# Optimization experiments

Measured on AMD Instinct MI355X. Metric: run time of the kernel, lower is better.

Reference implementation:

```python
import jax, jax.numpy as jnp
import numpy as np

B, F, S, D = 256, 8, 200, 64
H = 36  # hidden units per field
EPS = 1e-3  # Dice BN epsilon


def setup_inputs() -> dict:
    key0 = jax.random.key(0)
    ks = jax.random.split(key0, 8)
    query = jax.random.normal(ks[0], (B, F, D), dtype=jnp.float32)
    key = jax.random.normal(ks[1], (B, F, S, D), dtype=jnp.float32)
    sequence_num = jax.random.randint(ks[2], (B, F), 1, S + 1, dtype=jnp.int32)
    W_h = jax.random.normal(ks[3], (F, 3 * D, H), dtype=jnp.float32) * 0.05
    b_h = jnp.zeros((F, H), dtype=jnp.float32)
    alpha = jnp.zeros((F,), dtype=jnp.float32)
    W_o = jax.random.normal(ks[4], (F, H, 1), dtype=jnp.float32) * 0.05
    b_o = jnp.zeros((F, 1), dtype=jnp.float32)
    return {"query": query, "key": key, "W_h": W_h, "b_h": b_h,
            "alpha": alpha, "W_o": W_o, "b_o": b_o,
            "sequence_num": sequence_num, "training": 1}


def reference(query, key, W_h, b_h, alpha, W_o, b_o, sequence_num, training):
    # query: [B,F,D], key: [B,F,S,D]
    q = query[:, :, None, :]                      # broadcast instead of tile
    qb = jnp.broadcast_to(q, key.shape)           # [B,F,S,D]
    cat = jnp.concatenate([key, qb, q - key], axis=-1)  # [B,F,S,3D]
    # per-field Dense(36), vectorized across fields
    h = jnp.einsum('bfsc,fch->bfsh', cat, W_h) + b_h[None, :, None, :]
    # Dice: BatchNorm (no affine, training-mode batch stats over batch+seq per field/feature)
    mean = h.mean(axis=(0, 2), keepdims=True)
    var = h.var(axis=(0, 2), keepdims=True)
    p = jax.nn.sigmoid((h - mean) * jax.lax.rsqrt(var + EPS))
    h = (alpha[None, :, None, None] * (1.0 - p) + p) * h
    # per-field Dense(1) -> attention scores [B,F,S]
    scores = jnp.einsum('bfsh,fh->bfs', h, W_o[:, :, 0]) + b_o[None, :, 0, None]
    # mask invalid positions and softmax over sequence
    mask = jnp.arange(key.shape[2])[None, None, :] < sequence_num[:, :, None]
    scores = jnp.where(mask, scores, -jnp.inf)
    attn = jax.nn.softmax(scores, axis=-1)        # [B,F,S]
    # weighted sum over sequence -> [B,F,D]
    return jnp.einsum('bfs,bfsd->bfd', attn, key)
```

## Files before the change

### kernel.cpp

```cpp
#include <hip/hip_runtime.h>
#include <math.h>

#define NB 256
#define NF 8
#define NS 200
#define ND 64
#define NH 36
#define EPSV 1e-3f

#define WS_SUM 0
#define WS_SQ  288
#define WS_QT  1152

typedef __attribute__((ext_vector_type(8))) short short8;
typedef __attribute__((ext_vector_type(4))) float f32x4;
typedef __attribute__((ext_vector_type(4))) int int4v;

__device__ __forceinline__ unsigned short f32_to_bf16_rne(float x) {
    unsigned u = __float_as_uint(x);
    unsigned r = u + 0x7FFFu + ((u >> 16) & 1u);
    return (unsigned short)(r >> 16);
}
__device__ __forceinline__ short8 pack8(float4 a, float4 b) {
    int4v t;
    t[0] = (int)__builtin_amdgcn_perm(__float_as_uint(a.y), __float_as_uint(a.x), 0x07060302u);
    t[1] = (int)__builtin_amdgcn_perm(__float_as_uint(a.w), __float_as_uint(a.z), 0x07060302u);
    t[2] = (int)__builtin_amdgcn_perm(__float_as_uint(b.y), __float_as_uint(b.x), 0x07060302u);
    t[3] = (int)__builtin_amdgcn_perm(__float_as_uint(b.w), __float_as_uint(b.z), 0x07060302u);
    return __builtin_bit_cast(short8, t);
}

__global__ __launch_bounds__(128, 4) void k_stats(
    const float* __restrict__ query, const float* __restrict__ key,
    const float* __restrict__ W_h, const float* __restrict__ b_h,
    float* __restrict__ ws)
{
    const int blk = blockIdx.x;
    const int f = blk & (NF - 1);
    const int tid = threadIdx.x;
    const int lane = tid & 63, wv = tid >> 6;
    const int col = lane & 15, quad = lane >> 4;

    __shared__ __align__(16) unsigned short wkL[48 * 72];
    __shared__ float qsL[64];
    __shared__ float qtL[48];
    __shared__ float s1L[2][48], s2L[2][48];

    const float* Wf = W_h + (size_t)f * (3 * ND * NH);
    const float* kbase = key + (size_t)blk * (NS * ND);

    float4 cur[4], nxt[4];
    {
        const int s = min(16 * wv + col, NS - 1);
        const float4* p = (const float4*)(kbase + (size_t)s * ND + quad * 8);
        cur[0] = p[0]; cur[1] = p[1]; cur[2] = p[8]; cur[3] = p[9];
    }
    if (tid < 64) qsL[tid] = query[(size_t)blk * ND + tid];
    for (int i = tid; i < 48 * 64; i += 128) {
        int h = i >> 6, d = i & 63;
        float v = (h < NH) ? (Wf[d * NH + h] - Wf[(2 * ND + d) * NH + h]) : 0.f;
        wkL[h * 72 + d] = f32_to_bf16_rne(v);
    }
    __syncthreads();

    short8 bfr[3][2];
    #pragma unroll
    for (int nt = 0; nt < 3; ++nt)
        #pragma unroll
        for (int ks = 0; ks < 2; ++ks)
            bfr[nt][ks] = *(const short8*)&wkL[(nt * 16 + col) * 72 + ks * 32 + quad * 8];

    float s1[3] = {0.f, 0.f, 0.f}, s2[3] = {0.f, 0.f, 0.f};
    #pragma unroll
    for (int t = 0; t < 7; ++t) {
        const int mt = wv + 2 * t;
        if (t < 6) {
            const int sn = min(16 * (mt + 2) + col, NS - 1);
            const float4* p = (const float4*)(kbase + (size_t)sn * ND + quad * 8);
            nxt[0] = p[0]; nxt[1] = p[1]; nxt[2] = p[8]; nxt[3] = p[9];
        }
        const short8 fa = pack8(cur[0], cur[1]);
        const short8 fb = pack8(cur[2], cur[3]);
        const int base_s = 16 * mt + quad * 4;
        #pragma unroll
        for (int nt = 0; nt < 3; ++nt) {
            f32x4 acc = {0.f, 0.f, 0.f, 0.f};
            acc = __builtin_amdgcn_mfma_f32_16x16x32_bf16(fa, bfr[nt][0], acc, 0, 0, 0);
            acc = __builtin_amdgcn_mfma_f32_16x16x32_bf16(fb, bfr[nt][1], acc, 0, 0, 0);
            #pragma unroll
            for (int r = 0; r < 4; ++r) {
                const float v = (base_s + r < NS) ? acc[r] : 0.f;
                s1[nt] += v; s2[nt] += v * v;
            }
        }
        cur[0] = nxt[0]; cur[1] = nxt[1]; cur[2] = nxt[2]; cur[3] = nxt[3];
    }

    if (tid >= 64 && tid < 64 + NH) {
        const int h = tid - 64;
        float acc = b_h[f * NH + h];
        #pragma unroll 8
        for (int d = 0; d < ND; ++d)
            acc += qsL[d] * (Wf[(ND + d) * NH + h] + Wf[(2 * ND + d) * NH + h]);
        qtL[h] = acc;
        ws[WS_QT + (size_t)blk * 48 + h] = acc;
    }
    if (tid >= 64 + NH && tid < 64 + 48)
        ws[WS_QT + (size_t)blk * 48 + (tid - 64)] = 0.f;

    #pragma unroll
    for (int nt = 0; nt < 3; ++nt) {
        float a = s1[nt], c = s2[nt];
        a += __shfl_xor(a, 16, 64); a += __shfl_xor(a, 32, 64);
        c += __shfl_xor(c, 16, 64); c += __shfl_xor(c, 32, 64);
        if (quad == 0) { s1L[wv][nt * 16 + col] = a; s2L[wv][nt * 16 + col] = c; }
    }
    __syncthreads();
    if (tid < NH) {
        const float S1 = s1L[0][tid] + s1L[1][tid];
        const float S2 = s2L[0][tid] + s2L[1][tid];
        const float qt = qtL[tid];
        atomicAdd(&ws[WS_SUM + f * NH + tid], S1 + 200.f * qt);
        atomicAdd(&ws[WS_SQ  + f * NH + tid], S2 + 2.f * qt * S1 + 200.f * qt * qt);
    }
}

__global__ __launch_bounds__(128, 4) void k_attn(
    const float* __restrict__ key, const float* __restrict__ W_h,
    const float* __restrict__ alpha, const float* __restrict__ W_o,
    const float* __restrict__ b_o, const int* __restrict__ seqn,
    const float* __restrict__ ws, float* __restrict__ out)
{
    const int blk = blockIdx.x;
    const int f = blk & (NF - 1);
    const int tid = threadIdx.x;
    const int lane = tid & 63, wv = tid >> 6;
    const int col = lane & 15, quad = lane >> 4;

    __shared__ __align__(16) unsigned short wkL[48 * 72];
    __shared__ float swL[208];
    __shared__ float redA[2], redB[2];
    __shared__ float poutL[2][64];

    const float* Wf = W_h + (size_t)f * (3 * ND * NH);
    const float* kbase = key + (size_t)blk * (NS * ND);

    float4 cur[4], nxt[4];
    {
        const int s = min(16 * wv + col, NS - 1);
        const float4* p = (const float4*)(kbase + (size_t)s * ND + quad * 8);
        cur[0] = p[0]; cur[1] = p[1]; cur[2] = p[8]; cur[3] = p[9];
    }
    for (int i = tid; i < 48 * 64; i += 128) {
        int h = i >> 6, d = i & 63;
        float v = (h < NH) ? (Wf[d * NH + h] - Wf[(2 * ND + d) * NH + h]) : 0.f;
        wkL[h * 72 + d] = f32_to_bf16_rne(v);
    }
    __syncthreads();

    short8 bfr[3][2];
    #pragma unroll
    for (int nt = 0; nt < 3; ++nt)
        #pragma unroll
        for (int ks = 0; ks < 2; ++ks)
            bfr[nt][ks] = *(const short8*)&wkL[(nt * 16 + col) * 72 + ks * 32 + quad * 8];

    const float inv_n = 1.f / (float)(NB * NS);
    float qv[3], mn[3], iv[3], wo[3];
    #pragma unroll
    for (int nt = 0; nt < 3; ++nt) {
        const int hh = nt * 16 + col;
        const bool hv = hh < NH;
        const int hc = hv ? hh : 0;
        qv[nt] = ws[WS_QT + (size_t)blk * 48 + hh];
        const float sm = ws[WS_SUM + f * NH + hc];
        const float sq = ws[WS_SQ  + f * NH + hc];
        const float m = sm * inv_n;
        mn[nt] = m;
        iv[nt] = rsqrtf(fmaxf(sq * inv_n - m * m, 0.f) + EPSV);
        wo[nt] = hv ? W_o[f * NH + hh] : 0.f;
    }
    const float alf = alpha[f];
    const float bo = b_o[f];
    const int sq_n = seqn[blk];

    #pragma unroll
    for (int t = 0; t < 7; ++t) {
        const int mt = wv + 2 * t;
        if (t < 6) {
            const int sn = min(16 * (mt + 2) + col, NS - 1);
            const float4* p = (const float4*)(kbase + (size_t)sn * ND + quad * 8);
            nxt[0] = p[0]; nxt[1] = p[1]; nxt[2] = p[8]; nxt[3] = p[9];
        }
        const short8 fa = pack8(cur[0], cur[1]);
        const short8 fb = pack8(cur[2], cur[3]);
        float part[4] = {0.f, 0.f, 0.f, 0.f};
        #pragma unroll
        for (int nt = 0; nt < 3; ++nt) {
            f32x4 acc = {qv[nt], qv[nt], qv[nt], qv[nt]};
            acc = __builtin_amdgcn_mfma_f32_16x16x32_bf16(fa, bfr[nt][0], acc, 0, 0, 0);
            acc = __builtin_amdgcn_mfma_f32_16x16x32_bf16(fb, bfr[nt][1], acc, 0, 0, 0);
            #pragma unroll
            for (int r = 0; r < 4; ++r) {
                const float h = acc[r];
                const float pg = 1.f / (1.f + __expf(-(h - mn[nt]) * iv[nt]));
                part[r] += (alf + (1.f - alf) * pg) * h * wo[nt];
            }
        }
        #pragma unroll
        for (int r = 0; r < 4; ++r) {
            float v = part[r];
            v += __shfl_xor(v, 1, 64); v += __shfl_xor(v, 2, 64);
            v += __shfl_xor(v, 4, 64); v += __shfl_xor(v, 8, 64);
            const int srow = 16 * mt + quad * 4 + r;
            if (col == 0 && srow < NS) swL[srow] = v + bo;
        }
        cur[0] = nxt[0]; cur[1] = nxt[1]; cur[2] = nxt[2]; cur[3] = nxt[3];
    }
    __syncthreads();

    const int i2 = tid + 128;
    const float v1 = (tid < sq_n) ? swL[tid] : -1e30f;
    const float v2 = (i2 < NS && i2 < sq_n) ? swL[i2] : -1e30f;
    float m = fmaxf(v1, v2);
    m = fmaxf(m, __shfl_xor(m, 1, 64));  m = fmaxf(m, __shfl_xor(m, 2, 64));
    m = fmaxf(m, __shfl_xor(m, 4, 64));  m = fmaxf(m, __shfl_xor(m, 8, 64));
    m = fmaxf(m, __shfl_xor(m, 16, 64)); m = fmaxf(m, __shfl_xor(m, 32, 64));
    if (lane == 0) redA[wv] = m;
    __syncthreads();
    const float maxv = fmaxf(redA[0], redA[1]);
    const float e1 = (tid < sq_n) ? __expf(v1 - maxv) : 0.f;
    const float e2 = (i2 < NS && i2 < sq_n) ? __expf(v2 - maxv) : 0.f;
    float l = e1 + e2;
    l += __shfl_xor(l, 1, 64);  l += __shfl_xor(l, 2, 64);
    l += __shfl_xor(l, 4, 64);  l += __shfl_xor(l, 8, 64);
    l += __shfl_xor(l, 16, 64); l += __shfl_xor(l, 32, 64);
    if (lane == 0) redB[wv] = l;
    __syncthreads();
    const float isum = 1.f / (redB[0] + redB[1]);
    swL[tid] = e1 * isum;
    if (i2 < 208) swL[i2] = e2 * isum;
    __syncthreads();

    {
        const int d = lane;
        float acc = 0.f;
        const int s0 = wv * 100;
        #pragma unroll 10
        for (int s = s0; s < s0 + 100; ++s)
            acc += swL[s] * kbase[(size_t)s * ND + d];
        poutL[wv][d] = acc;
    }
    __syncthreads();
    if (tid < 64)
        out[(size_t)blk * ND + tid] = poutL[0][tid] + poutL[1][tid];
}

extern "C" void kernel_launch(void* const* d_in, const int* in_sizes, int n_in,
                              void* d_out, int out_size, void* d_ws, size_t ws_size,
                              hipStream_t stream) {
    const float* query = (const float*)d_in[0];
    const float* key   = (const float*)d_in[1];
    const float* W_h   = (const float*)d_in[2];
    const float* b_h   = (const float*)d_in[3];
    const float* alpha = (const float*)d_in[4];
    const float* W_o   = (const float*)d_in[5];
    const float* b_o   = (const float*)d_in[6];
    const int*   seqn  = (const int*)d_in[7];
    float* out = (float*)d_out;
    float* ws  = (float*)d_ws;

    hipMemsetAsync(ws, 0, 576 * sizeof(float), stream);
    k_stats<<<NB * NF, 128, 0, stream>>>(query, key, W_h, b_h, ws);
    k_attn<<<NB * NF, 128, 0, stream>>>(key, W_h, alpha, W_o, b_o, seqn, ws, out);
}
```

Before: 225.7 us.

## Stage key tile in LDS as bf16, widen blocks, replace atomics with reduce kernel

After: 222.1 us. No clear change (-1.6%).

```diff
diff --git a/kernel.cpp b/kernel.cpp
--- a/kernel.cpp
+++ b/kernel.cpp
@@ -10,53 +10,63 @@
 
 #define WS_SUM 0
 #define WS_SQ  288
-#define WS_QT  1152
+#define WS_QT  4096
+#define WS_P   102400
 
 typedef __attribute__((ext_vector_type(8))) short short8;
 typedef __attribute__((ext_vector_type(4))) float f32x4;
-typedef __attribute__((ext_vector_type(4))) int int4v;
 
 __device__ __forceinline__ unsigned short f32_to_bf16_rne(float x) {
     unsigned u = __float_as_uint(x);
     unsigned r = u + 0x7FFFu + ((u >> 16) & 1u);
     return (unsigned short)(r >> 16);
 }
-__device__ __forceinline__ short8 pack8(float4 a, float4 b) {
-    int4v t;
-    t[0] = (int)__builtin_amdgcn_perm(__float_as_uint(a.y), __float_as_uint(a.x), 0x07060302u);
-    t[1] = (int)__builtin_amdgcn_perm(__float_as_uint(a.w), __float_as_uint(a.z), 0x07060302u);
-    t[2] = (int)__builtin_amdgcn_perm(__float_as_uint(b.y), __float_as_uint(b.x), 0x07060302u);
-    t[3] = (int)__builtin_amdgcn_perm(__float_as_uint(b.w), __float_as_uint(b.z), 0x07060302u);
-    return __builtin_bit_cast(short8, t);
-}
-
-__global__ __launch_bounds__(128, 4) void k_stats(
+__device__ __forceinline__ unsigned pack2(float x, float y) {
+    return __builtin_amdgcn_perm(__float_as_uint(y), __float_as_uint(x), 0x07060302u);
+}
+
+__device__ __forceinline__ void stage_key(const float* kbase, unsigned short* kL,
+                                          int tid, int lane, int wv) {
+    const float4* kb4 = (const float4*)kbase;
+    const int base = wv * 800;
+    #pragma unroll
+    for (int j = 0; j < 13; ++j) {
+        const int idx = base + j * 64 + lane;
+        const bool ok = (j < 12) | (lane < 32);
+        const float4 v = kb4[ok ? idx : base];
+        if (ok) {
+            const int r = idx >> 4, dc = idx & 15;
+            unsigned t0 = pack2(v.x, v.y), t1 = pack2(v.z, v.w);
+            uint2 u; u.x = t0; u.y = t1;
+            *(uint2*)&kL[r * 72 + dc * 4] = u;
+        }
+    }
+    for (int i = tid; i < 288; i += 256) ((unsigned*)&kL[200 * 72])[i] = 0u;
+}
+
+__global__ __launch_bounds__(256, 4) void k_stats(
     const float* __restrict__ query, const float* __restrict__ key,
     const float* __restrict__ W_h, const float* __restrict__ b_h,
     float* __restrict__ ws)
 {
     const int blk = blockIdx.x;
     const int f = blk & (NF - 1);
+    const int b = blk >> 3;
     const int tid = threadIdx.x;
     const int lane = tid & 63, wv = tid >> 6;
     const int col = lane & 15, quad = lane >> 4;
 
+    __shared__ __align__(16) unsigned short kL[208 * 72];
     __shared__ __align__(16) unsigned short wkL[48 * 72];
-    __shared__ float qsL[64];
-    __shared__ float qtL[48];
-    __shared__ float s1L[2][48], s2L[2][48];
+    __shared__ float qsL[64], qtL[48];
+    __shared__ float s1L[4][48], s2L[4][48];
 
     const float* Wf = W_h + (size_t)f * (3 * ND * NH);
     const float* kbase = key + (size_t)blk * (NS * ND);
 
-    float4 cur[4], nxt[4];
-    {
-        const int s = min(16 * wv + col, NS - 1);
-        const float4* p = (const float4*)(kbase + (size_t)s * ND + quad * 8);
-        cur[0] = p[0]; cur[1] = p[1]; cur[2] = p[8]; cur[3] = p[9];
-    }
+    stage_key(kbase, kL, tid, lane, wv);
     if (tid < 64) qsL[tid] = query[(size_t)blk * ND + tid];
-    for (int i = tid; i < 48 * 64; i += 128) {
+    for (int i = tid; i < 48 * 64; i += 256) {
         int h = i >> 6, d = i & 63;
         float v = (h < NH) ? (Wf[d * NH + h] - Wf[(2 * ND + d) * NH + h]) : 0.f;
         wkL[h * 72 + d] = f32_to_bf16_rne(v);
@@ -71,16 +81,9 @@
             bfr[nt][ks] = *(const short8*)&wkL[(nt * 16 + col) * 72 + ks * 32 + quad * 8];
 
     float s1[3] = {0.f, 0.f, 0.f}, s2[3] = {0.f, 0.f, 0.f};
-    #pragma unroll
-    for (int t = 0; t < 7; ++t) {
-        const int mt = wv + 2 * t;
-        if (t < 6) {
-            const int sn = min(16 * (mt + 2) + col, NS - 1);
-            const float4* p = (const float4*)(kbase + (size_t)sn * ND + quad * 8);
-            nxt[0] = p[0]; nxt[1] = p[1]; nxt[2] = p[8]; nxt[3] = p[9];
-        }
-        const short8 fa = pack8(cur[0], cur[1]);
-        const short8 fb = pack8(cur[2], cur[3]);
+    for (int mt = wv; mt < 13; mt += 4) {
+        const short8 fa = *(const short8*)&kL[(16 * mt + col) * 72 + quad * 8];
+        const short8 fb = *(const short8*)&kL[(16 * mt + col) * 72 + 32 + quad * 8];
         const int base_s = 16 * mt + quad * 4;
         #pragma unroll
         for (int nt = 0; nt < 3; ++nt) {
@@ -93,7 +96,6 @@
                 s1[nt] += v; s2[nt] += v * v;
             }
         }
-        cur[0] = nxt[0]; cur[1] = nxt[1]; cur[2] = nxt[2]; cur[3] = nxt[3];
     }
 
     if (tid >= 64 && tid < 64 + NH) {
@@ -117,15 +119,30 @@
     }
     __syncthreads();
     if (tid < NH) {
-        const float S1 = s1L[0][tid] + s1L[1][tid];
-        const float S2 = s2L[0][tid] + s2L[1][tid];
+        const float S1 = s1L[0][tid] + s1L[1][tid] + s1L[2][tid] + s1L[3][tid];
+        const float S2 = s2L[0][tid] + s2L[1][tid] + s2L[2][tid] + s2L[3][tid];
         const float qt = qtL[tid];
-        atomicAdd(&ws[WS_SUM + f * NH + tid], S1 + 200.f * qt);
-        atomicAdd(&ws[WS_SQ  + f * NH + tid], S2 + 2.f * qt * S1 + 200.f * qt * qt);
-    }
-}
-
-__global__ __launch_bounds__(128, 4) void k_attn(
+        ws[WS_P + (size_t)(f * 72 + tid) * 256 + b]      = S1 + 200.f * qt;
+        ws[WS_P + (size_t)(f * 72 + 36 + tid) * 256 + b] = S2 + 2.f * qt * S1 + 200.f * qt * qt;
+    }
+}
+
+__global__ __launch_bounds__(64) void k_reduce(float* __restrict__ ws) {
+    const int j = blockIdx.x;
+    const int lane = threadIdx.x;
+    const float4 v = ((const float4*)&ws[WS_P + (size_t)j * 256])[lane];
+    float s = v.x + v.y + v.z + v.w;
+    s += __shfl_xor(s, 1, 64);  s += __shfl_xor(s, 2, 64);
+    s += __shfl_xor(s, 4, 64);  s += __shfl_xor(s, 8, 64);
+    s += __shfl_xor(s, 16, 64); s += __shfl_xor(s, 32, 64);
+    if (lane == 0) {
+        const int f = j / 72, jj = j % 72;
+        if (jj < NH) ws[WS_SUM + f * NH + jj] = s;
+        else         ws[WS_SQ  + f * NH + (jj - NH)] = s;
+    }
+}
+
+__global__ __launch_bounds__(256, 4) void k_attn(
     const float* __restrict__ key, const float* __restrict__ W_h,
     const float* __restrict__ alpha, const float* __restrict__ W_o,
     const float* __restrict__ b_o, const int* __restrict__ seqn,
@@ -137,21 +154,17 @@
     const int lane = tid & 63, wv = tid >> 6;
     const int col = lane & 15, quad = lane >> 4;
 
+    __shared__ __align__(16) unsigned short kL[208 * 72];
     __shared__ __align__(16) unsigned short wkL[48 * 72];
     __shared__ float swL[208];
-    __shared__ float redA[2], redB[2];
-    __shared__ float poutL[2][64];
+    __shared__ float redA[4], redB[4];
+    __shared__ float poutL[8][64];
 
     const float* Wf = W_h + (size_t)f * (3 * ND * NH);
     const float* kbase = key + (size_t)blk * (NS * ND);
 
-    float4 cur[4], nxt[4];
-    {
-        const int s = min(16 * wv + col, NS - 1);
-        const float4* p = (const float4*)(kbase + (size_t)s * ND + quad * 8);
-        cur[0] = p[0]; cur[1] = p[1]; cur[2] = p[8]; cur[3] = p[9];
-    }
-    for (int i = tid; i < 48 * 64; i += 128) {
+    stage_key(kbase, kL, tid, lane, wv);
+    for (int i = tid; i < 48 * 64; i += 256) {
         int h = i >> 6, d = i & 63;
         float v = (h < NH) ? (Wf[d * NH + h] - Wf[(2 * ND + d) * NH + h]) : 0.f;
         wkL[h * 72 + d] = f32_to_bf16_rne(v);
@@ -184,16 +197,9 @@
     const float bo = b_o[f];
     const int sq_n = seqn[blk];
 
-    #pragma unroll
-    for (int t = 0; t < 7; ++t) {
-        const int mt = wv + 2 * t;
-        if (t < 6) {
-            const int sn = min(16 * (mt + 2) + col, NS - 1);
-            const float4* p = (const float4*)(kbase + (size_t)sn * ND + quad * 8);
-            nxt[0] = p[0]; nxt[1] = p[1]; nxt[2] = p[8]; nxt[3] = p[9];
-        }
-        const short8 fa = pack8(cur[0], cur[1]);
-        const short8 fb = pack8(cur[2], cur[3]);
+    for (int mt = wv; mt < 13; mt += 4) {
+        const short8 fa = *(const short8*)&kL[(16 * mt + col) * 72 + quad * 8];
+        const short8 fb = *(const short8*)&kL[(16 * mt + col) * 72 + 32 + quad * 8];
         float part[4] = {0.f, 0.f, 0.f, 0.f};
         #pragma unroll
         for (int nt = 0; nt < 3; ++nt) {
@@ -215,45 +221,51 @@
             const int srow = 16 * mt + quad * 4 + r;
             if (col == 0 && srow < NS) swL[srow] = v + bo;
         }
-        cur[0] = nxt[0]; cur[1] = nxt[1]; cur[2] = nxt[2]; cur[3] = nxt[3];
-    }
-    __syncthreads();
-
-    const int i2 = tid + 128;
-    const float v1 = (tid < sq_n) ? swL[tid] : -1e30f;
-    const float v2 = (i2 < NS && i2 < sq_n) ? swL[i2] : -1e30f;
-    float m = fmaxf(v1, v2);
+    }
+    __syncthreads();
+
+    const bool valid = (tid < NS) && (tid < sq_n);
+    const float sc = valid ? swL[tid] : -1e30f;
+    float m = sc;
     m = fmaxf(m, __shfl_xor(m, 1, 64));  m = fmaxf(m, __shfl_xor(m, 2, 64));
     m = fmaxf(m, __shfl_xor(m, 4, 64));  m = fmaxf(m, __shfl_xor(m, 8, 64));
     m = fmaxf(m, __shfl_xor(m, 16, 64)); m = fmaxf(m, __shfl_xor(m, 32, 64));
     if (lane == 0) redA[wv] = m;
     __syncthreads();
-    const float maxv = fmaxf(redA[0], redA[1]);
-    const float e1 = (tid < sq_n) ? __expf(v1 - maxv) : 0.f;
-    const float e2 = (i2 < NS && i2 < sq_n) ? __expf(v2 - maxv) : 0.f;
-    float l = e1 + e2;
+    const float maxv = fmaxf(fmaxf(redA[0], redA[1]), fmaxf(redA[2], redA[3]));
+    const float e = valid ? __expf(sc - maxv) : 0.f;
+    float l = e;
     l += __shfl_xor(l, 1, 64);  l += __shfl_xor(l, 2, 64);
     l += __shfl_xor(l, 4, 64);  l += __shfl_xor(l, 8, 64);
     l += __shfl_xor(l, 16, 64); l += __shfl_xor(l, 32, 64);
     if (lane == 0) redB[wv] = l;
     __syncthreads();
-    const float isum = 1.f / (redB[0] + redB[1]);
-    swL[tid] = e1 * isum;
-    if (i2 < 208) swL[i2] = e2 * isum;
+    const float isum = 1.f / (redB[0] + redB[1] + redB[2] + redB[3]);
+    if (tid < NS) swL[tid] = e * isum;
     __syncthreads();
 
     {
-        const int d = lane;
-        float acc = 0.f;
-        const int s0 = wv * 100;
-        #pragma unroll 10
-        for (int s = s0; s < s0 + 100; ++s)
-            acc += swL[s] * kbase[(size_t)s * ND + d];
-        poutL[wv][d] = acc;
-    }
-    __syncthreads();
-    if (tid < 64)
-        out[(size_t)blk * ND + tid] = poutL[0][tid] + poutL[1][tid];
+        const int g = wv * 2 + (lane >> 5);
+        const int c = lane & 31;
+        float a0 = 0.f, a1 = 0.f;
+        const int s0 = g * 25;
+        #pragma unroll 5
+        for (int s = s0; s < s0 + 25; ++s) {
+            const unsigned w2 = *(const unsigned*)&kL[s * 72 + 2 * c];
+            const float wgt = swL[s];
+            a0 += wgt * __uint_as_float(w2 << 16);
+            a1 += wgt * __uint_as_float(w2 & 0xFFFF0000u);
+        }
+        poutL[g][2 * c]     = a0;
+        poutL[g][2 * c + 1] = a1;
+    }
+    __syncthreads();
+    if (tid < 64) {
+        float o = 0.f;
+        #pragma unroll
+        for (int g = 0; g < 8; ++g) o += poutL[g][tid];
+        out[(size_t)blk * ND + tid] = o;
+    }
 }
 
 extern "C" void kernel_launch(void* const* d_in, const int* in_sizes, int n_in,
@@ -270,7 +282,7 @@
     float* out = (float*)d_out;
     float* ws  = (float*)d_ws;
 
-    hipMemsetAsync(ws, 0, 576 * sizeof(float), stream);
-    k_stats<<<NB * NF, 128, 0, stream>>>(query, key, W_h, b_h, ws);
-    k_attn<<<NB * NF, 128, 0, stream>>>(key, W_h, alpha, W_o, b_o, seqn, ws, out);
-}
+    k_stats<<<NB * NF, 256, 0, stream>>>(query, key, W_h, b_h, ws);
+    k_reduce<<<576, 64, 0, stream>>>(ws);
+    k_attn<<<NB * NF, 256, 0, stream>>>(key, W_h, alpha, W_o, b_o, seqn, ws, out);
+}
```
